# Optimization experiments

Measured on AMD Instinct MI355X. Metric: run time of the kernel, lower is better.

Reference implementation:

```python
import jax, jax.numpy as jnp
import numpy as np

N = 20000
E = 160000
H = 8          # heads
D = 96         # head_dim (768 // 8)
C = H * D      # 768 hidden channels
G = 256        # num graphs
NUM_CLASSES = 32
SLOPE = 0.2    # GATv2 LeakyReLU negative slope


def layer_norm(x, w, b, eps=1e-5):
    mu = jnp.mean(x, axis=-1, keepdims=True)
    var = jnp.mean(jnp.square(x - mu), axis=-1, keepdims=True)
    return (x - mu) * jax.lax.rsqrt(var + eps) * w + b


def gatv2_layer(x, src, dst, Wl, bl, Wr, br, att, bias):
    # x: [N, C]; src/dst: [E'] with self loops included
    xl = (x @ Wl + bl).reshape(N, H, D)   # source projection
    xr = (x @ Wr + br).reshape(N, H, D)   # target projection
    e = xl[src] + xr[dst]                 # [E', H, D] edge gather
    e = jnp.where(e > 0, e, SLOPE * e)    # LeakyReLU
    logits = jnp.einsum('ehd,hd->eh', e, att)  # [E', H]
    m = jax.ops.segment_max(logits, dst, num_segments=N)
    ex = jnp.exp(logits - m[dst])
    s = jax.ops.segment_sum(ex, dst, num_segments=N)
    alpha = ex / s[dst]                   # segment softmax over in-edges
    out = jax.ops.segment_sum(alpha[:, :, None] * xl[src], dst, num_segments=N)
    return out.reshape(N, C) + bias


def setup_inputs() -> dict:
    key = jax.random.key(0)
    ks = jax.random.split(key, 24)
    x = jax.random.normal(ks[0], (N, 768), jnp.float32)
    edge_index = jax.random.randint(ks[1], (2, E), 0, N, jnp.int64)
    batch = jnp.sort(jax.random.randint(ks[2], (N,), 0, G, jnp.int64))
    sc = 1.0 / np.sqrt(C)
    p = {
        'x': x, 'edge_index': edge_index, 'batch': batch,
        'w_in': jax.random.normal(ks[3], (768, C), jnp.float32) * sc,
        'b_in': jnp.zeros((C,), jnp.float32),
        'Wl': jax.random.normal(ks[4], (3, C, C), jnp.float32) * sc,
        'bl': jnp.zeros((3, C), jnp.float32),
        'Wr': jax.random.normal(ks[5], (3, C, C), jnp.float32) * sc,
        'br': jnp.zeros((3, C), jnp.float32),
        'att': jax.random.normal(ks[6], (3, H, D), jnp.float32) * (1.0 / np.sqrt(D)),
        'gat_bias': jnp.zeros((3, C), jnp.float32),
        'ln_w': jnp.ones((3, C), jnp.float32),
        'ln_b': jnp.zeros((3, C), jnp.float32),
        'out_ln_w': jnp.ones((3 * C,), jnp.float32),
        'out_ln_b': jnp.zeros((3 * C,), jnp.float32),
        'w_out': jax.random.normal(ks[7], (3 * C, NUM_CLASSES), jnp.float32) * (1.0 / np.sqrt(3 * C)),
        'b_out': jnp.zeros((NUM_CLASSES,), jnp.float32),
    }
    return p


def reference(x, edge_index, batch, w_in, b_in, Wl, bl, Wr, br, att, gat_bias,
              ln_w, ln_b, out_ln_w, out_ln_b, w_out, b_out):
    # add self loops (PyG add_self_loops=True)
    loops = jnp.arange(N, dtype=edge_index.dtype)
    src = jnp.concatenate([edge_index[0], loops])
    dst = jnp.concatenate([edge_index[1], loops])

    h = x @ w_in + b_in
    jumps = []
    for l in range(3):
        a = gatv2_layer(h, src, dst, Wl[l], bl[l], Wr[l], br[l], att[l], gat_bias[l])
        h = layer_norm(a + h, ln_w[l], ln_b[l])
        h = jax.nn.gelu(h, approximate=False)
        jumps.append(h)
    hc = jnp.concatenate(jumps, axis=-1)  # JumpingKnowledge 'cat' -> [N, 3C]

    # global mean pool over graphs
    sums = jax.ops.segment_sum(hc, batch, num_segments=G)
    cnt = jax.ops.segment_sum(jnp.ones((N, 1), hc.dtype), batch, num_segments=G)
    pooled = sums / jnp.maximum(cnt, 1.0)

    out = layer_norm(pooled, out_ln_w, out_ln_b)
    return out @ w_out + b_out
```

## Files before the change

### kernel.cpp

```cpp
#include <hip/hip_runtime.h>

#define N_NODES 20000
#define N_EDGES 160000
#define CH      768
#define CH3     2304
#define NGRAPH  256
#define NCLS    32

typedef __bf16 bf16v8 __attribute__((ext_vector_type(8)));
typedef float  f32x4  __attribute__((ext_vector_type(4)));

__device__ __forceinline__ float b2f(ushort u) {
    union { float f; unsigned u; } x; x.u = ((unsigned)u) << 16; return x.f;
}
__device__ __forceinline__ ushort f2b(float f) {
    union { float f; unsigned u; } x; x.f = f;
    unsigned r = x.u + 0x7FFFu + ((x.u >> 16) & 1u);
    return (ushort)(r >> 16);
}
__device__ __forceinline__ void load12(const ushort* __restrict__ p, float* o) {
    const ushort4* q = (const ushort4*)p;
    ushort4 a = q[0], b = q[1], c = q[2];
    o[0]=b2f(a.x); o[1]=b2f(a.y); o[2]=b2f(a.z); o[3]=b2f(a.w);
    o[4]=b2f(b.x); o[5]=b2f(b.y); o[6]=b2f(b.z); o[7]=b2f(b.w);
    o[8]=b2f(c.x); o[9]=b2f(c.y); o[10]=b2f(c.z); o[11]=b2f(c.w);
}
__device__ __forceinline__ void load12f(const float* __restrict__ p, float* o) {
    const float4* q = (const float4*)p;
    float4 a = q[0], b = q[1], c = q[2];
    o[0]=a.x; o[1]=a.y; o[2]=a.z; o[3]=a.w;
    o[4]=b.x; o[5]=b.y; o[6]=b.z; o[7]=b.w;
    o[8]=c.x; o[9]=c.y; o[10]=c.z; o[11]=c.w;
}
__device__ __forceinline__ void async_copy16(void* lds, const void* gp) {
    __builtin_amdgcn_global_load_lds((const void __attribute__((address_space(1)))*)gp,
                                     (void __attribute__((address_space(3)))*)lds, 16, 0, 0);
}

__global__ void cvt_x_kernel(const float* __restrict__ src, ushort* __restrict__ dst, int n4) {
    int i = blockIdx.x * 256 + threadIdx.x;
    if (i >= n4) return;
    float4 v = ((const float4*)src)[i];
    ushort4 o; o.x = f2b(v.x); o.y = f2b(v.y); o.z = f2b(v.z); o.w = f2b(v.w);
    ((ushort4*)dst)[i] = o;
}

__global__ void transpose_cvt768(const float* __restrict__ in, ushort* __restrict__ out) {
    __shared__ float tile[32][33];
    int bx = blockIdx.x * 32, by = blockIdx.y * 32;
    int tx = threadIdx.x, ty = threadIdx.y;
    #pragma unroll
    for (int i = ty; i < 32; i += 8) tile[i][tx] = in[(size_t)(by + i) * CH + bx + tx];
    __syncthreads();
    #pragma unroll
    for (int i = ty; i < 32; i += 8) out[(size_t)(bx + i) * CH + by + tx] = f2b(tile[tx][i]);
}

__global__ void init_deg_kernel(int* deg, int n) {
    int i = blockIdx.x * 256 + threadIdx.x;
    if (i < n) deg[i] = 1;
}
__global__ void count_kernel(const int* __restrict__ dst, int* __restrict__ deg, int e) {
    int i = blockIdx.x * 256 + threadIdx.x;
    if (i < e) atomicAdd(&deg[dst[i]], 1);
}
__global__ __launch_bounds__(1024) void scan_kernel(const int* __restrict__ deg,
                                                    int* __restrict__ rowptr, int n) {
    __shared__ int part[1024];
    int t = threadIdx.x;
    const int chunk = (n + 1023) / 1024;
    int base = t * chunk;
    int s = 0;
    for (int i = 0; i < chunk; ++i) { int idx = base + i; if (idx < n) s += deg[idx]; }
    part[t] = s; __syncthreads();
    for (int off = 1; off < 1024; off <<= 1) {
        int v = (t >= off) ? part[t - off] : 0;
        __syncthreads();
        part[t] += v;
        __syncthreads();
    }
    int run = (t == 0) ? 0 : part[t - 1];
    for (int i = 0; i < chunk; ++i) {
        int idx = base + i;
        if (idx < n) { rowptr[idx] = run; run += deg[idx]; }
    }
    if (t == 1023) rowptr[n] = part[1023];
}
__global__ void selfloop_kernel(const int* __restrict__ rowptr, int* __restrict__ csrc,
                                int* __restrict__ cursor, int n) {
    int i = blockIdx.x * 256 + threadIdx.x;
    if (i < n) { int p = rowptr[i]; csrc[p] = i; cursor[i] = p + 1; }
}
__global__ void scatter_kernel(const int* __restrict__ src, const int* __restrict__ dst,
                               int* __restrict__ cursor, int* __restrict__ csrc, int e) {
    int i = blockIdx.x * 256 + threadIdx.x;
    if (i < e) { int p = atomicAdd(&cursor[dst[i]], 1); csrc[p] = src[i]; }
}
__global__ void gcount_kernel(const int* __restrict__ batch, int* __restrict__ gcount, int n) {
    int i = blockIdx.x * 256 + threadIdx.x;
    if (i < n) atomicAdd(&gcount[batch[i]], 1);
}
__global__ __launch_bounds__(256) void gscan_kernel(const int* __restrict__ gcount,
                                                    int* __restrict__ gstart) {
    __shared__ int p[256];
    int t = threadIdx.x;
    p[t] = gcount[t]; __syncthreads();
    for (int off = 1; off < 256; off <<= 1) {
        int v = (t >= off) ? p[t - off] : 0;
        __syncthreads();
        p[t] += v;
        __syncthreads();
    }
    gstart[t] = p[t] - gcount[t];
    if (t == 255) gstart[256] = p[255];
}

__global__ __launch_bounds__(256) void gemm_bf16_kernel(
    const ushort* __restrict__ A, int lda,
    const ushort* __restrict__ Bt,
    const float* __restrict__ biasA, const float* __restrict__ biasB, int nsplit,
    ushort* __restrict__ C, int ldc, int M) {
    __shared__ __bf16 As[128 * 32];
    __shared__ __bf16 Bs[128 * 32];
    int tid = threadIdx.x;
    int wave = tid >> 6, lane = tid & 63;
    int wr = wave >> 1, wc = wave & 1;

    int bid = blockIdx.y * gridDim.x + blockIdx.x;
    int pf = 8 * gridDim.y;
    int p  = bid / pf;
    int rem = bid - p * pf;
    int rp = min(8, (int)gridDim.x - p * 8);
    int row_t = p * 8 + rem % rp;
    int col_t = rem / rp;
    int row0 = row_t * 128, col0 = col_t * 128;

    int c1 = wave * 64 + lane, c2 = c1 + 256;
    int ar1 = min(row0 + (c1 >> 2), M - 1), ak1 = (c1 & 3) * 8;
    int ar2 = min(row0 + (c2 >> 2), M - 1), ak2 = (c2 & 3) * 8;
    int br1 = col0 + (c1 >> 2), br2 = col0 + (c2 >> 2);
    const ushort* a1 = A + (size_t)ar1 * lda + ak1;
    const ushort* a2 = A + (size_t)ar2 * lda + ak2;
    const ushort* b1 = Bt + (size_t)br1 * CH + ak1;
    const ushort* b2 = Bt + (size_t)br2 * CH + ak2;
    __bf16* asb1 = As + (wave * 64) * 8;
    __bf16* asb2 = As + (256 + wave * 64) * 8;
    __bf16* bsb1 = Bs + (wave * 64) * 8;
    __bf16* bsb2 = Bs + (256 + wave * 64) * 8;

    f32x4 acc[4][4] = {};
    int l16 = lane & 15, lq = lane >> 4;

    for (int k0 = 0; k0 < CH; k0 += 32) {
        async_copy16(asb1, a1 + k0);
        async_copy16(asb2, a2 + k0);
        async_copy16(bsb1, b1 + k0);
        async_copy16(bsb2, b2 + k0);
        __syncthreads();
        bf16v8 av[4], bv[4];
        #pragma unroll
        for (int i = 0; i < 4; ++i)
            av[i] = *(const bf16v8*)(As + ((wr * 64 + i * 16 + l16) * 32 + lq * 8));
        #pragma unroll
        for (int j = 0; j < 4; ++j)
            bv[j] = *(const bf16v8*)(Bs + ((wc * 64 + j * 16 + l16) * 32 + lq * 8));
        #pragma unroll
        for (int i = 0; i < 4; ++i)
            #pragma unroll
            for (int j = 0; j < 4; ++j)
                acc[i][j] = __builtin_amdgcn_mfma_f32_16x16x32_bf16(av[i], bv[j], acc[i][j], 0, 0, 0);
        __syncthreads();
    }
    #pragma unroll
    for (int i = 0; i < 4; ++i) {
        int mbase = row0 + wr * 64 + i * 16 + lq * 4;
        #pragma unroll
        for (int j = 0; j < 4; ++j) {
            int col = col0 + wc * 64 + j * 16 + l16;
            float bb = (col < nsplit) ? biasA[col] : biasB[col - nsplit];
            #pragma unroll
            for (int r = 0; r < 4; ++r) {
                int mm = mbase + r;
                if (mm < M) C[(size_t)mm * ldc + col] = f2b(acc[i][j][r] + bb);
            }
        }
    }
}

__global__ __launch_bounds__(256) void gat_node_kernel(
    const ushort* __restrict__ xlxr,
    const ushort* __restrict__ hin, int ldh,
    const int* __restrict__ rowptr, const int* __restrict__ csrc,
    const float* __restrict__ att, const float* __restrict__ gbias,
    const float* __restrict__ lnw, const float* __restrict__ lnb,
    ushort* __restrict__ hout, int nn) {
    int wv = threadIdx.x >> 6, lane = threadIdx.x & 63;
    int n = blockIdx.x * 4 + wv;
    if (n >= nn) return;
    int c0 = lane * 12;
    float attv[12], xr[12], acc[12];
    load12f(att + c0, attv);
    load12(xlxr + (size_t)n * 1536 + CH + c0, xr);
    #pragma unroll
    for (int j = 0; j < 12; ++j) acc[j] = 0.f;
    float m = -1e30f, ssum = 0.f;
    int rs = rowptr[n], re = rowptr[n + 1];
    for (int e = rs; e < re; ++e) {
        int s = csrc[e];
        float xl[12];
        load12(xlxr + (size_t)s * 1536 + c0, xl);
        float dot = 0.f;
        #pragma unroll
        for (int j = 0; j < 12; ++j) {
            float v = xl[j] + xr[j];
            v = (v > 0.f) ? v : 0.2f * v;
            dot = fmaf(v, attv[j], dot);
        }
        dot += __shfl_xor(dot, 1);
        dot += __shfl_xor(dot, 2);
        dot += __shfl_xor(dot, 4);
        float nm = fmaxf(m, dot);
        float sc = __expf(m - nm);
        float ex = __expf(dot - nm);
        ssum = ssum * sc + ex;
        #pragma unroll
        for (int j = 0; j < 12; ++j) acc[j] = fmaf(acc[j], sc, ex * xl[j]);
        m = nm;
    }
    float inv = 1.f / ssum;
    float hres[12], gb[12], tv[12];
    load12(hin + (size_t)n * ldh + c0, hres);
    load12f(gbias + c0, gb);
    float lsum = 0.f;
    #pragma unroll
    for (int j = 0; j < 12; ++j) { tv[j] = acc[j] * inv + gb[j] + hres[j]; lsum += tv[j]; }
    #pragma unroll
    for (int o = 1; o < 64; o <<= 1) lsum += __shfl_xor(lsum, o);
    float mu = lsum * (1.f / 768.f);
    float lsq = 0.f;
    #pragma unroll
    for (int j = 0; j < 12; ++j) { float d = tv[j] - mu; lsq = fmaf(d, d, lsq); }
    #pragma unroll
    for (int o = 1; o < 64; o <<= 1) lsq += __shfl_xor(lsq, o);
    float rstd = rsqrtf(lsq * (1.f / 768.f) + 1e-5f);
    float wv12[12], bv12[12];
    load12f(lnw + c0, wv12);
    load12f(lnb + c0, bv12);
    ushort* op = hout + (size_t)n * CH3 + c0;
    #pragma unroll
    for (int j = 0; j < 12; ++j) {
        float y = (tv[j] - mu) * rstd * wv12[j] + bv12[j];
        float g = 0.5f * y * (1.f + erff(y * 0.70710678118f));
        op[j] = f2b(g);
    }
}

__global__ __launch_bounds__(256) void pool_kernel(const ushort* __restrict__ hc,
                                                   const int* __restrict__ gstart,
                                                   float* __restrict__ pooled) {
    int g = blockIdx.x;
    int c = blockIdx.y * 256 + threadIdx.x;
    int s = gstart[g], e = gstart[g + 1];
    const ushort* p = hc + (size_t)s * CH3 + c;
    float a = 0.f;
    for (int n = s; n < e; ++n) { a += b2f(*p); p += CH3; }
    pooled[(size_t)g * CH3 + c] = a * (1.f / (float)max(e - s, 1));
}

__global__ __launch_bounds__(256) void head_kernel(const float* __restrict__ pooled,
                                                   const float* __restrict__ olnw,
                                                   const float* __restrict__ olnb,
                                                   const float* __restrict__ wout,
                                                   const float* __restrict__ bout,
                                                   float* __restrict__ outp) {
    __shared__ float row[CH3];
    __shared__ float red[8];
    __shared__ float parts[8][32];
    int g = blockIdx.x, t = threadIdx.x;
    int lane = t & 63, wv = t >> 6;
    float s = 0.f;
    for (int c = t; c < CH3; c += 256) { float v = pooled[(size_t)g * CH3 + c]; row[c] = v; s += v; }
    #pragma unroll
    for (int o = 1; o < 64; o <<= 1) s += __shfl_xor(s, o);
    if (lane == 0) red[wv] = s;
    __syncthreads();
    float mu = (red[0] + red[1] + red[2] + red[3]) * (1.f / (float)CH3);
    float q = 0.f;
    for (int c = t; c < CH3; c += 256) { float d = row[c] - mu; q += d * d; }
    #pragma unroll
    for (int o = 1; o < 64; o <<= 1) q += __shfl_xor(q, o);
    if (lane == 0) red[4 + wv] = q;
    __syncthreads();
    float rstd = rsqrtf((red[4] + red[5] + red[6] + red[7]) * (1.f / (float)CH3) + 1e-5f);
    for (int c = t; c < CH3; c += 256)
        row[c] = (row[c] - mu) * rstd * olnw[c] + olnb[c];
    __syncthreads();
    int j = t & 31, slice = t >> 5;
    float a = 0.f;
    int cb = slice * (CH3 / 8);
    for (int c = cb; c < cb + CH3 / 8; ++c) a += row[c] * wout[(size_t)c * 32 + j];
    parts[slice][j] = a;
    __syncthreads();
    if (t < 32) {
        float r = bout[t];
        #pragma unroll
        for (int si = 0; si < 8; ++si) r += parts[si][t];
        outp[(size_t)g * 32 + t] = r;
    }
}

extern "C" void kernel_launch(void* const* d_in, const int* in_sizes, int n_in,
                              void* d_out, int out_size, void* d_ws, size_t ws_size,
                              hipStream_t stream) {
    const float* x     = (const float*)d_in[0];
    const int*   ei    = (const int*)d_in[1];
    const int*   batch = (const int*)d_in[2];
    const float* w_in  = (const float*)d_in[3];
    const float* b_in  = (const float*)d_in[4];
    const float* Wl    = (const float*)d_in[5];
    const float* bl    = (const float*)d_in[6];
    const float* Wr    = (const float*)d_in[7];
    const float* br    = (const float*)d_in[8];
    const float* att   = (const float*)d_in[9];
    const float* gbias = (const float*)d_in[10];
    const float* lnw   = (const float*)d_in[11];
    const float* lnb   = (const float*)d_in[12];
    const float* olnw  = (const float*)d_in[13];
    const float* olnb  = (const float*)d_in[14];
    const float* wout  = (const float*)d_in[15];
    const float* bout  = (const float*)d_in[16];

    char* ws = (char*)d_ws;
    size_t off = 0;
    auto alloc = [&](size_t bytes) -> void* {
        void* p = ws + off;
        off = (off + bytes + 255) & ~(size_t)255;
        return p;
    };
    ushort* h0     = (ushort*)alloc((size_t)N_NODES * CH * 2);
    ushort* hc     = (ushort*)alloc((size_t)N_NODES * CH3 * 2);
    ushort* xlxr   = (ushort*)alloc((size_t)N_NODES * 1536 * 2);
    ushort* wt_in  = (ushort*)alloc((size_t)CH * CH * 2);
    ushort* wt_l   = (ushort*)alloc((size_t)3 * 1536 * CH * 2);
    int*    deg    = (int*)alloc((size_t)N_NODES * 4);
    int*    rowptr = (int*)alloc((size_t)(N_NODES + 1) * 4);
    int*    cursor = (int*)alloc((size_t)N_NODES * 4);
    int*    csrc   = (int*)alloc((size_t)(N_EDGES + N_NODES) * 4);
    int*    gcount = (int*)alloc(256 * 4);
    int*    gstart = (int*)alloc(257 * 4);
    float*  pooled = (float*)alloc((size_t)NGRAPH * CH3 * 4);
    if (off > ws_size) return;

    ushort* xc = hc;

    cvt_x_kernel<<<(N_NODES * CH / 4 + 255) / 256, 256, 0, stream>>>(x, xc, N_NODES * CH / 4);
    dim3 tb32(32, 8), tg24(24, 24);
    transpose_cvt768<<<tg24, tb32, 0, stream>>>(w_in, wt_in);
    for (int l = 0; l < 3; ++l) {
        transpose_cvt768<<<tg24, tb32, 0, stream>>>(Wl + (size_t)l * CH * CH,
                                                    wt_l + (size_t)l * 1536 * CH);
        transpose_cvt768<<<tg24, tb32, 0, stream>>>(Wr + (size_t)l * CH * CH,
                                                    wt_l + (size_t)l * 1536 * CH + (size_t)CH * CH);
    }

    int nb = (N_NODES + 255) / 256, eb = (N_EDGES + 255) / 256;
    init_deg_kernel<<<nb, 256, 0, stream>>>(deg, N_NODES);
    count_kernel<<<eb, 256, 0, stream>>>(ei + N_EDGES, deg, N_EDGES);
    scan_kernel<<<1, 1024, 0, stream>>>(deg, rowptr, N_NODES);
    selfloop_kernel<<<nb, 256, 0, stream>>>(rowptr, csrc, cursor, N_NODES);
    scatter_kernel<<<eb, 256, 0, stream>>>(ei, ei + N_EDGES, cursor, csrc, N_EDGES);
    hipMemsetAsync(gcount, 0, 256 * 4, stream);
    gcount_kernel<<<nb, 256, 0, stream>>>(batch, gcount, N_NODES);
    gscan_kernel<<<1, 256, 0, stream>>>(gcount, gstart);

    gemm_bf16_kernel<<<dim3(157, 6), 256, 0, stream>>>(
        xc, CH, wt_in, b_in, b_in, CH, h0, CH, N_NODES);

    for (int l = 0; l < 3; ++l) {
        const ushort* hprev = (l == 0) ? h0 : (hc + (size_t)(l - 1) * CH);
        int ldh = (l == 0) ? CH : CH3;
        gemm_bf16_kernel<<<dim3(157, 12), 256, 0, stream>>>(
            hprev, ldh, wt_l + (size_t)l * 1536 * CH,
            bl + (size_t)l * CH, br + (size_t)l * CH, CH,
            xlxr, 1536, N_NODES);
        gat_node_kernel<<<N_NODES / 4, 256, 0, stream>>>(
            xlxr, hprev, ldh, rowptr, csrc,
            att + (size_t)l * CH, gbias + (size_t)l * CH,
            lnw + (size_t)l * CH, lnb + (size_t)l * CH,
            hc + (size_t)l * CH, N_NODES);
    }

    pool_kernel<<<dim3(NGRAPH, CH3 / 256), 256, 0, stream>>>(hc, gstart, pooled);
    head_kernel<<<NGRAPH, 256, 0, stream>>>(pooled, olnw, olnb, wout, bout, (float*)d_out);
}
```

Before: 792.7 us.

## Merge weight transposes and count kernels; dual-stream online softmax in GAT

Replaces the seven per-matrix transpose launches with a single 3D-grid launch, and folds the graph-count and degree-count kernels plus a memset into shared init and count kernels, cutting launch overhead. The GAT node kernel now handles two edges per iteration with two independent online-softmax accumulators, merged at the end. This exposes more memory-level parallelism for the gathered source rows, at the cost of higher register pressure.

Result: faster. 754.3 us (-4.8%).

```diff
diff --git a/kernel.cpp b/kernel.cpp
--- a/kernel.cpp
+++ b/kernel.cpp
@@ -45,8 +45,21 @@
     ((ushort4*)dst)[i] = o;
 }
 
-__global__ void transpose_cvt768(const float* __restrict__ in, ushort* __restrict__ out) {
+__global__ void transpose_cvt_all(const float* __restrict__ w_in,
+                                  const float* __restrict__ Wl,
+                                  const float* __restrict__ Wr,
+                                  ushort* __restrict__ wt_in,
+                                  ushort* __restrict__ wt_l) {
     __shared__ float tile[32][33];
+    int z = blockIdx.z;
+    const float* in;
+    ushort* out;
+    if (z == 0) { in = w_in; out = wt_in; }
+    else {
+        int l = (z - 1) >> 1, isr = (z - 1) & 1;
+        in  = (isr ? Wr : Wl) + (size_t)l * CH * CH;
+        out = wt_l + (size_t)l * 1536 * CH + (size_t)isr * CH * CH;
+    }
     int bx = blockIdx.x * 32, by = blockIdx.y * 32;
     int tx = threadIdx.x, ty = threadIdx.y;
     #pragma unroll
@@ -56,13 +69,16 @@
     for (int i = ty; i < 32; i += 8) out[(size_t)(bx + i) * CH + by + tx] = f2b(tile[tx][i]);
 }
 
-__global__ void init_deg_kernel(int* deg, int n) {
+__global__ void init_kernel(int* deg, int* gcount, int n) {
     int i = blockIdx.x * 256 + threadIdx.x;
     if (i < n) deg[i] = 1;
-}
-__global__ void count_kernel(const int* __restrict__ dst, int* __restrict__ deg, int e) {
+    if (i < 256) gcount[i] = 0;
+}
+__global__ void count_both_kernel(const int* __restrict__ dst, int* __restrict__ deg, int e,
+                                  const int* __restrict__ batch, int* __restrict__ gcount, int n) {
     int i = blockIdx.x * 256 + threadIdx.x;
     if (i < e) atomicAdd(&deg[dst[i]], 1);
+    if (i < n) atomicAdd(&gcount[batch[i]], 1);
 }
 __global__ __launch_bounds__(1024) void scan_kernel(const int* __restrict__ deg,
                                                     int* __restrict__ rowptr, int n) {
@@ -95,10 +111,6 @@
                                int* __restrict__ cursor, int* __restrict__ csrc, int e) {
     int i = blockIdx.x * 256 + threadIdx.x;
     if (i < e) { int p = atomicAdd(&cursor[dst[i]], 1); csrc[p] = src[i]; }
-}
-__global__ void gcount_kernel(const int* __restrict__ batch, int* __restrict__ gcount, int n) {
-    int i = blockIdx.x * 256 + threadIdx.x;
-    if (i < n) atomicAdd(&gcount[batch[i]], 1);
 }
 __global__ __launch_bounds__(256) void gscan_kernel(const int* __restrict__ gcount,
                                                     int* __restrict__ gstart) {
@@ -198,42 +210,75 @@
     int n = blockIdx.x * 4 + wv;
     if (n >= nn) return;
     int c0 = lane * 12;
-    float attv[12], xr[12], acc[12];
+    float attv[12], xr[12], acc1[12], acc2[12];
     load12f(att + c0, attv);
     load12(xlxr + (size_t)n * 1536 + CH + c0, xr);
     #pragma unroll
-    for (int j = 0; j < 12; ++j) acc[j] = 0.f;
-    float m = -1e30f, ssum = 0.f;
+    for (int j = 0; j < 12; ++j) { acc1[j] = 0.f; acc2[j] = 0.f; }
+    float m1 = -1e30f, s1 = 0.f, m2 = -1e30f, s2 = 0.f;
     int rs = rowptr[n], re = rowptr[n + 1];
-    for (int e = rs; e < re; ++e) {
-        int s = csrc[e];
-        float xl[12];
-        load12(xlxr + (size_t)s * 1536 + c0, xl);
-        float dot = 0.f;
+    int e = rs;
+    for (; e + 1 < re; e += 2) {
+        int sa = csrc[e], sb = csrc[e + 1];
+        float xa[12], xb[12];
+        load12(xlxr + (size_t)sa * 1536 + c0, xa);
+        load12(xlxr + (size_t)sb * 1536 + c0, xb);
+        float da = 0.f, db = 0.f;
         #pragma unroll
         for (int j = 0; j < 12; ++j) {
-            float v = xl[j] + xr[j];
-            v = (v > 0.f) ? v : 0.2f * v;
-            dot = fmaf(v, attv[j], dot);
+            float va = xa[j] + xr[j]; va = (va > 0.f) ? va : 0.2f * va;
+            float vb = xb[j] + xr[j]; vb = (vb > 0.f) ? vb : 0.2f * vb;
+            da = fmaf(va, attv[j], da);
+            db = fmaf(vb, attv[j], db);
         }
-        dot += __shfl_xor(dot, 1);
-        dot += __shfl_xor(dot, 2);
-        dot += __shfl_xor(dot, 4);
-        float nm = fmaxf(m, dot);
-        float sc = __expf(m - nm);
-        float ex = __expf(dot - nm);
-        ssum = ssum * sc + ex;
-        #pragma unroll
-        for (int j = 0; j < 12; ++j) acc[j] = fmaf(acc[j], sc, ex * xl[j]);
-        m = nm;
-    }
+        da += __shfl_xor(da, 1); db += __shfl_xor(db, 1);
+        da += __shfl_xor(da, 2); db += __shfl_xor(db, 2);
+        da += __shfl_xor(da, 4); db += __shfl_xor(db, 4);
+        float nm1 = fmaxf(m1, da), nm2 = fmaxf(m2, db);
+        float sc1 = __expf(m1 - nm1), sc2 = __expf(m2 - nm2);
+        float ex1 = __expf(da - nm1), ex2 = __expf(db - nm2);
+        s1 = s1 * sc1 + ex1;
+        s2 = s2 * sc2 + ex2;
+        #pragma unroll
+        for (int j = 0; j < 12; ++j) {
+            acc1[j] = fmaf(acc1[j], sc1, ex1 * xa[j]);
+            acc2[j] = fmaf(acc2[j], sc2, ex2 * xb[j]);
+        }
+        m1 = nm1; m2 = nm2;
+    }
+    if (e < re) {
+        int sa = csrc[e];
+        float xa[12];
+        load12(xlxr + (size_t)sa * 1536 + c0, xa);
+        float da = 0.f;
+        #pragma unroll
+        for (int j = 0; j < 12; ++j) {
+            float va = xa[j] + xr[j]; va = (va > 0.f) ? va : 0.2f * va;
+            da = fmaf(va, attv[j], da);
+        }
+        da += __shfl_xor(da, 1);
+        da += __shfl_xor(da, 2);
+        da += __shfl_xor(da, 4);
+        float nm = fmaxf(m1, da);
+        float sc = __expf(m1 - nm), ex = __expf(da - nm);
+        s1 = s1 * sc + ex;
+        #pragma unroll
+        for (int j = 0; j < 12; ++j) acc1[j] = fmaf(acc1[j], sc, ex * xa[j]);
+        m1 = nm;
+    }
+    float M = fmaxf(m1, m2);
+    float w1 = __expf(m1 - M), w2 = __expf(m2 - M);
+    float ssum = s1 * w1 + s2 * w2;
     float inv = 1.f / ssum;
     float hres[12], gb[12], tv[12];
     load12(hin + (size_t)n * ldh + c0, hres);
     load12f(gbias + c0, gb);
     float lsum = 0.f;
     #pragma unroll
-    for (int j = 0; j < 12; ++j) { tv[j] = acc[j] * inv + gb[j] + hres[j]; lsum += tv[j]; }
+    for (int j = 0; j < 12; ++j) {
+        tv[j] = (acc1[j] * w1 + acc2[j] * w2) * inv + gb[j] + hres[j];
+        lsum += tv[j];
+    }
     #pragma unroll
     for (int o = 1; o < 64; o <<= 1) lsum += __shfl_xor(lsum, o);
     float mu = lsum * (1.f / 768.f);
@@ -354,23 +399,14 @@
     ushort* xc = hc;
 
     cvt_x_kernel<<<(N_NODES * CH / 4 + 255) / 256, 256, 0, stream>>>(x, xc, N_NODES * CH / 4);
-    dim3 tb32(32, 8), tg24(24, 24);
-    transpose_cvt768<<<tg24, tb32, 0, stream>>>(w_in, wt_in);
-    for (int l = 0; l < 3; ++l) {
-        transpose_cvt768<<<tg24, tb32, 0, stream>>>(Wl + (size_t)l * CH * CH,
-                                                    wt_l + (size_t)l * 1536 * CH);
-        transpose_cvt768<<<tg24, tb32, 0, stream>>>(Wr + (size_t)l * CH * CH,
-                                                    wt_l + (size_t)l * 1536 * CH + (size_t)CH * CH);
-    }
+    transpose_cvt_all<<<dim3(24, 24, 7), dim3(32, 8), 0, stream>>>(w_in, Wl, Wr, wt_in, wt_l);
 
     int nb = (N_NODES + 255) / 256, eb = (N_EDGES + 255) / 256;
-    init_deg_kernel<<<nb, 256, 0, stream>>>(deg, N_NODES);
-    count_kernel<<<eb, 256, 0, stream>>>(ei + N_EDGES, deg, N_EDGES);
+    init_kernel<<<nb, 256, 0, stream>>>(deg, gcount, N_NODES);
+    count_both_kernel<<<eb, 256, 0, stream>>>(ei + N_EDGES, deg, N_EDGES, batch, gcount, N_NODES);
     scan_kernel<<<1, 1024, 0, stream>>>(deg, rowptr, N_NODES);
     selfloop_kernel<<<nb, 256, 0, stream>>>(rowptr, csrc, cursor, N_NODES);
     scatter_kernel<<<eb, 256, 0, stream>>>(ei, ei + N_EDGES, cursor, csrc, N_EDGES);
-    hipMemsetAsync(gcount, 0, 256 * 4, stream);
-    gcount_kernel<<<nb, 256, 0, stream>>>(batch, gcount, N_NODES);
     gscan_kernel<<<1, 256, 0, stream>>>(gcount, gstart);
 
     gemm_bf16_kernel<<<dim3(157, 6), 256, 0, stream>>>(
```
